# Optimization experiments

Measured on AMD Instinct MI355X. Metric: run time of the kernel, lower is better.

The kernel has to match this reference:

```python
import jax, jax.numpy as jnp
import numpy as np

NT, NRV, NR = 100000, 200000, 300000  # tile / road_vertex / road node counts
E = 400000                             # edges per edge type
B, H, P, A = 64, 128, 64, 512          # graphs, hidden, player_state_dim, action_dim


def _gat(h_src, h_dst, src, dst, W, a_s, a_d, b, n_dst):
    # PyG GATConv, heads=1, shared lin for src/dst, no self loops (bipartite)
    hs = h_src @ W                      # [Ns, H]
    hd = h_dst @ W                      # [Nd, H]
    e = jax.nn.leaky_relu((hs @ a_s)[src] + (hd @ a_d)[dst], 0.2)  # [E]
    m = jax.ops.segment_max(e, dst, num_segments=n_dst)
    w = jnp.exp(e - m[dst])
    denom = jax.ops.segment_sum(w, dst, num_segments=n_dst)
    alpha = w / jnp.maximum(denom[dst], 1e-16)                      # segment softmax
    out = jax.ops.segment_sum(alpha[:, None] * hs[src], dst, num_segments=n_dst)
    return out + b


def _mean_pool(x, batch, nb):
    s = jax.ops.segment_sum(x, batch, num_segments=nb)
    c = jax.ops.segment_sum(jnp.ones((x.shape[0],), x.dtype), batch, num_segments=nb)
    return s / jnp.maximum(c, 1.0)[:, None]


def setup_inputs():
    ks = iter(jax.random.split(jax.random.key(0), 64))
    f32 = jnp.float32

    def lin(i, o):
        return (jax.random.normal(next(ks), (i, o), f32) / np.float32(np.sqrt(i)))

    d = {}
    d['x_tile'] = jax.random.normal(next(ks), (NT, 8), f32)
    d['x_rv'] = jax.random.normal(next(ks), (NRV, 13), f32)
    d['x_road'] = jax.random.normal(next(ks), (NR, 4), f32)
    d['x_player'] = jax.random.normal(next(ks), (B, P), f32)
    # node encoders
    d['enc_t_W'] = lin(8, H);  d['enc_t_b'] = jnp.zeros((H,), f32)
    d['enc_rv_W'] = lin(13, H); d['enc_rv_b'] = jnp.zeros((H,), f32)
    d['enc_r_W'] = lin(4, H);  d['enc_r_b'] = jnp.zeros((H,), f32)
    # six GAT convs
    for name in ['rv2t', 't2rv', 'r2rv', 'rv2r', 't2r', 'r2t']:
        d[name + '_W'] = lin(H, H)
        d[name + '_as'] = jax.random.normal(next(ks), (H,), f32) * 0.1
        d[name + '_ad'] = jax.random.normal(next(ks), (H,), f32) * 0.1
        d[name + '_b'] = jnp.zeros((H,), f32)
    # player MLP + output head (input: 3H pooled + H player)
    d['fc1_W'] = lin(P, H); d['fc1_b'] = jnp.zeros((H,), f32)
    d['fc2_W'] = lin(H, H); d['fc2_b'] = jnp.zeros((H,), f32)
    d['out_W'] = lin(4 * H, A); d['out_b'] = jnp.zeros((A,), f32)
    # edges (src bounded by source-type count, dst by dest-type count)
    ri = lambda n, hi: jax.random.randint(n, (E,), 0, hi, jnp.int32)
    d['e_rv2t_src'] = ri(next(ks), NRV); d['e_rv2t_dst'] = ri(next(ks), NT)
    d['e_t2rv_src'] = ri(next(ks), NT);  d['e_t2rv_dst'] = ri(next(ks), NRV)
    d['e_r2rv_src'] = ri(next(ks), NR);  d['e_r2rv_dst'] = ri(next(ks), NRV)
    d['e_rv2r_src'] = ri(next(ks), NRV); d['e_rv2r_dst'] = ri(next(ks), NR)
    d['e_t2r_src'] = ri(next(ks), NT);   d['e_t2r_dst'] = ri(next(ks), NR)
    d['e_r2t_src'] = ri(next(ks), NR);   d['e_r2t_dst'] = ri(next(ks), NT)
    # batch assignment per node type
    d['batch_tile'] = jnp.sort(jax.random.randint(next(ks), (NT,), 0, B, jnp.int32))
    d['batch_rv'] = jnp.sort(jax.random.randint(next(ks), (NRV,), 0, B, jnp.int32))
    d['batch_road'] = jnp.sort(jax.random.randint(next(ks), (NR,), 0, B, jnp.int32))
    return d


def reference(x_tile, x_rv, x_road, x_player,
              enc_t_W, enc_t_b, enc_rv_W, enc_rv_b, enc_r_W, enc_r_b,
              rv2t_W, rv2t_as, rv2t_ad, rv2t_b,
              t2rv_W, t2rv_as, t2rv_ad, t2rv_b,
              r2rv_W, r2rv_as, r2rv_ad, r2rv_b,
              rv2r_W, rv2r_as, rv2r_ad, rv2r_b,
              t2r_W, t2r_as, t2r_ad, t2r_b,
              r2t_W, r2t_as, r2t_ad, r2t_b,
              fc1_W, fc1_b, fc2_W, fc2_b, out_W, out_b,
              e_rv2t_src, e_rv2t_dst, e_t2rv_src, e_t2rv_dst,
              e_r2rv_src, e_r2rv_dst, e_rv2r_src, e_rv2r_dst,
              e_t2r_src, e_t2r_dst, e_r2t_src, e_r2t_dst,
              batch_tile, batch_rv, batch_road):
    # node encoders
    h_t = x_tile @ enc_t_W + enc_t_b
    h_rv = x_rv @ enc_rv_W + enc_rv_b
    h_r = x_road @ enc_r_W + enc_r_b
    # hetero GAT, aggr='sum' over edge types per destination node type
    o_t = (_gat(h_rv, h_t, e_rv2t_src, e_rv2t_dst, rv2t_W, rv2t_as, rv2t_ad, rv2t_b, NT)
           + _gat(h_r, h_t, e_r2t_src, e_r2t_dst, r2t_W, r2t_as, r2t_ad, r2t_b, NT))
    o_rv = (_gat(h_t, h_rv, e_t2rv_src, e_t2rv_dst, t2rv_W, t2rv_as, t2rv_ad, t2rv_b, NRV)
            + _gat(h_r, h_rv, e_r2rv_src, e_r2rv_dst, r2rv_W, r2rv_as, r2rv_ad, r2rv_b, NRV))
    o_r = (_gat(h_rv, h_r, e_rv2r_src, e_rv2r_dst, rv2r_W, rv2r_as, rv2r_ad, rv2r_b, NR)
           + _gat(h_t, h_r, e_t2r_src, e_t2r_dst, t2r_W, t2r_as, t2r_ad, t2r_b, NR))
    # global mean pool per node type, concat -> [B, 3H]
    x_all = jnp.concatenate([_mean_pool(o_t, batch_tile, B),
                             _mean_pool(o_rv, batch_rv, B),
                             _mean_pool(o_r, batch_road, B)], axis=1)
    # player branch
    p = jax.nn.relu(x_player @ fc1_W + fc1_b)
    p = jax.nn.relu(p @ fc2_W + fc2_b)
    x = jnp.concatenate([x_all, p], axis=1)  # [B, 4H]
    return x @ out_W + out_b                 # [B, A]
```

## Files before the change

kernel.cpp:

```cpp
#include <hip/hip_runtime.h>


constexpr int kNT = 100000, kNRV = 200000, kNR = 300000, kE = 400000;
constexpr int kEq   = kE / 4;
constexpr int kSLOT = 1088;
constexpr int kNBB  = 1536;
constexpr int kBPS  = 192;
constexpr int kTOTD = 1200000;

constexpr long long OFF_C    = 0;
constexpr long long OFF_VS   = 13056;
constexpr long long OFF_VD   = 13176;
constexpr long long OFF_BD   = 13296;
constexpr long long OFF_PS   = 13512;
constexpr long long OFF_XCAT = 22216;
constexpr long long OFF_LS16 = 54984;
constexpr long long OFF_LD16 = 654984;
constexpr long long OFF_W16  = 1254984;
constexpr long long OFF_DN   = 2454984;
constexpr long long OFF_XR   = 3654984;
constexpr long long OFF_BID  = 6254984;
constexpr long long OFF_PB   = 6554984;

__constant__ const int kLSB[6]  = {0, 200000, 300000, 600000, 800000, 900000};
__constant__ const int kDRB[6]  = {0, 100000, 300000, 500000, 800000, 1100000};
__constant__ const int kDLEN[6] = {100000, 200000, 200000, 300000, 300000, 100000};
__constant__ const int cSlotEt[8]  = {1, 2, 4, 5, 0, 0, 3, 3};
__constant__ const int cSlotLo[8]  = {0, 0, 0, 0, 0, 100000, 0, 100000};
__constant__ const int cSlotHi[8]  = {1 << 30, 1 << 30, 1 << 30, 1 << 30,
                                      100000, 200000, 100000, 200000};
__constant__ const int cSlotCnt[8] = {1, 1, 1, 1, 1, 0, 1, 0};

__device__ __forceinline__ int lowb(const int* a, int n, int v) {
  int lo = 0, hi = n;
  while (lo < hi) { int mid = (lo + hi) >> 1; if (a[mid] < v) lo = mid + 1; else hi = mid; }
  return lo;
}

__global__ __launch_bounds__(256) void precompute_kernel(
    const float* encW_t, const float* encb_t,
    const float* encW_rv, const float* encb_rv,
    const float* encW_r, const float* encb_r,
    const float* W0, const float* as0, const float* ad0,
    const float* W1, const float* as1, const float* ad1,
    const float* W2, const float* as2, const float* ad2,
    const float* W3, const float* as3, const float* ad3,
    const float* W4, const float* as4, const float* ad4,
    const float* W5, const float* as5, const float* ad5,
    const int* bt, const int* brv, const int* br,
    float* Cws, float* vsw, float* vdw, int* BD)
{
  int tid = threadIdx.x;
  if (blockIdx.x == 24) {
    if (tid < 3 * 65) {
      int tt = tid / 65, q = tid - tt * 65;
      const int* ba = (tt == 0) ? bt : (tt == 1 ? brv : br);
      int N = (tt == 0) ? kNT : (tt == 1 ? kNRV : kNR);
      BD[tt * 72 + q] = lowb(ba, N, q);
    }
    return;
  }
  const float* encW[3] = {encW_t, encW_rv, encW_r};
  const float* encb[3] = {encb_t, encb_rv, encb_r};
  const int    Ks[3]   = {8, 13, 4};
  const float* Wv[6]  = {W0, W1, W2, W3, W4, W5};
  const float* asv[6] = {as0, as1, as2, as3, as4, as5};
  const float* adv[6] = {ad0, ad1, ad2, ad3, ad4, ad5};
  const int srcT[6] = {1, 0, 2, 1, 0, 2};
  const int dstT[6] = {0, 1, 1, 2, 2, 0};

  int et = blockIdx.x >> 2;
  int jc = blockIdx.x & 3;
  int st = srcT[et], dt = dstT[et];
  const float* eW = encW[st];
  const float* eB = encb[st];
  int K = Ks[st];
  const float* W = Wv[et];

  float* Cslot = Cws + et * 2176;
  for (int idx = tid; idx < (K + 1) * 32; idx += 256) {
    int r = idx >> 5, jj = idx & 31;
    int j = jc * 32 + jj;
    const float* row = (r < K) ? (eW + r * 128) : eB;
    float acc = 0.f;
    for (int m = 0; m < 128; ++m) acc += row[m] * W[m * 128 + j];
    Cslot[(r < K) ? (r * 128 + j) : (2048 + j)] = acc;
  }

  if (jc == 0) {
    __shared__ float us[128], wvs[128];
    const float* a_s = asv[et];
    const float* a_d = adv[et];
    if (tid < 128) {
      float acc = 0.f;
      for (int j = 0; j < 128; ++j) acc += W[tid * 128 + j] * a_s[j];
      us[tid] = acc;
    } else {
      int m = tid - 128;
      float acc = 0.f;
      for (int j = 0; j < 128; ++j) acc += W[m * 128 + j] * a_d[j];
      wvs[m] = acc;
    }
    __syncthreads();
    if (tid <= K) {
      const float* row = (tid < K) ? (eW + tid * 128) : eB;
      float acc = 0.f;
      for (int m = 0; m < 128; ++m) acc += row[m] * us[m];
      vsw[et * 20 + (tid < K ? tid : 16)] = acc;
    }
    int KD = Ks[dt];
    if (tid >= 32 && tid <= 32 + KD) {
      int k = tid - 32;
      const float* row = (k < KD) ? (encW[dt] + k * 128) : encb[dt];
      float acc = 0.f;
      for (int m = 0; m < 128; ++m) acc += row[m] * wvs[m];
      vdw[et * 20 + (k < KD ? k : 16)] = acc;
    }
  }
}

template <int K, int RH>
__device__ __forceinline__ void prep_one(
    const float* __restrict__ xr, unsigned char b,
    const float* __restrict__ vsA, const float* __restrict__ vsB,
    const float* __restrict__ vdA, const float* __restrict__ vdB,
    _Float16* lsA, _Float16* lsB, _Float16* ldA, _Float16* ldB,
    float* dnA, float* dnB, unsigned char* bidA, unsigned char* bidB,
    _Float16* xrec)
{
  float a0 = 0.f, a1 = 0.f, a2 = 0.f, a3 = 0.f;
#pragma unroll
  for (int k = 0; k < K; ++k) {
    float xv = xr[k];
    a0 += xv * vsA[k]; a1 += xv * vsB[k];
    a2 += xv * vdA[k]; a3 += xv * vdB[k];
    xrec[k] = (_Float16)xv;
  }
#pragma unroll
  for (int k = K; k < RH; ++k) xrec[k] = (_Float16)0.f;
  *lsA = (_Float16)(a0 + vsA[16]);
  *lsB = (_Float16)(a1 + vsB[16]);
  *ldA = (_Float16)(a2 + vdA[16]);
  *ldB = (_Float16)(a3 + vdB[16]);
  *dnA = 0.f;
  *dnB = 0.f;
  *bidA = b;
  *bidB = b;
}

__global__ __launch_bounds__(256) void prep_kernel(
    const float* __restrict__ x_t, const float* __restrict__ x_rv,
    const float* __restrict__ x_r,
    const int* __restrict__ bt, const int* __restrict__ brv,
    const int* __restrict__ br,
    const float* __restrict__ vsw, const float* __restrict__ vdw,
    _Float16* __restrict__ LS16, _Float16* __restrict__ LD16,
    float* __restrict__ DN, unsigned char* __restrict__ BID,
    _Float16* __restrict__ XR)
{
  int n = blockIdx.x * 256 + threadIdx.x;
  if (n >= kNT + kNRV + kNR) return;
  if (n < kNT) {
    prep_one<8, 8>(x_t + n * 8, (unsigned char)bt[n],
                   vsw + 1 * 20, vsw + 4 * 20, vdw + 0 * 20, vdw + 5 * 20,
                   LS16 + 200000 + n, LS16 + 800000 + n,
                   LD16 + 0 + n, LD16 + 1100000 + n,
                   DN + 0 + n, DN + 1100000 + n,
                   BID + 0 + n, BID + 1100000 + n,
                   XR + (long long)n * 8);
  } else if (n < kNT + kNRV) {
    int m = n - kNT;
    prep_one<13, 16>(x_rv + m * 13, (unsigned char)brv[m],
                     vsw + 0 * 20, vsw + 3 * 20, vdw + 1 * 20, vdw + 2 * 20,
                     LS16 + 0 + m, LS16 + 600000 + m,
                     LD16 + 100000 + m, LD16 + 300000 + m,
                     DN + 100000 + m, DN + 300000 + m,
                     BID + 100000 + m, BID + 300000 + m,
                     XR + 800000 + (long long)m * 16);
  } else {
    int m = n - kNT - kNRV;
    prep_one<4, 4>(x_r + m * 4, (unsigned char)br[m],
                   vsw + 2 * 20, vsw + 5 * 20, vdw + 3 * 20, vdw + 4 * 20,
                   LS16 + 300000 + m, LS16 + 900000 + m,
                   LD16 + 500000 + m, LD16 + 800000 + m,
                   DN + 500000 + m, DN + 800000 + m,
                   BID + 500000 + m, BID + 800000 + m,
                   XR + 4000000 + (long long)m * 4);
  }
}

__global__ __launch_bounds__(256) void passA_kernel(
    const int* s0, const int* s1, const int* s2,
    const int* s3, const int* s4, const int* s5,
    const int* d0, const int* d1, const int* d2,
    const int* d3, const int* d4, const int* d5,
    const _Float16* __restrict__ LS16, const _Float16* __restrict__ LD16,
    float* __restrict__ DN, _Float16* __restrict__ W16)
{
  int slot = blockIdx.x & 7;
  int blk = blockIdx.x >> 3;
  for (int i = blk * 256 + (int)threadIdx.x; i < 75000; i += kBPS * 256) {
    int gq = slot * 75000 + i;
    int et = gq / 100000;
    int q = gq - et * 100000;
    const int* sp; const int* dp;
    switch (et) {
      case 0: sp = s0; dp = d0; break;
      case 1: sp = s1; dp = d1; break;
      case 2: sp = s2; dp = d2; break;
      case 3: sp = s3; dp = d3; break;
      case 4: sp = s4; dp = d4; break;
      default: sp = s5; dp = d5; break;
    }
    int lsb = kLSB[et], drb = kDRB[et];
    int4 ss = ((const int4*)sp)[q];
    int4 dd = ((const int4*)dp)[q];
    int sa[4] = {ss.x, ss.y, ss.z, ss.w};
    int da[4] = {dd.x, dd.y, dd.z, dd.w};
    union { float2 f; _Float16 h[4]; } WU;
    float wa[4];
#pragma unroll
    for (int j = 0; j < 4; ++j) {
      float t = (float)LS16[lsb + sa[j]] + (float)LD16[drb + da[j]];
      t = t > 0.f ? t : 0.2f * t;
      _Float16 h = (_Float16)__expf(t);
      WU.h[j] = h;
      wa[j] = (float)h;
    }
    ((float2*)(W16 + (long long)et * kE))[q] = WU.f;
#pragma unroll
    for (int j = 0; j < 4; ++j) unsafeAtomicAdd(&DN[drb + da[j]], wa[j]);
  }
}

__global__ __launch_bounds__(256) void pack_kernel(
    const float* __restrict__ DN, const unsigned char* __restrict__ BID,
    unsigned* __restrict__ DNu)
{
  int j = blockIdx.x * 256 + threadIdx.x;
  if (j >= kTOTD) return;
  float dn = DN[j];
  unsigned u = 0u;
  if (dn > 0.f)
    u = (__float_as_uint(1.f / dn) & ~63u) | (unsigned)BID[j];
  DNu[j] = u;
}

template <int RH>
__device__ __forceinline__ void loadX(const _Float16* __restrict__ xp, float* xv) {
  if constexpr (RH == 4) {
    union { uint2 u; _Float16 h[4]; } U;
    U.u = *(const uint2*)xp;
#pragma unroll
    for (int k = 0; k < RH; ++k) xv[k] = (float)U.h[k];
  } else if constexpr (RH == 8) {
    union { uint4 u; _Float16 h[8]; } U;
    U.u = *(const uint4*)xp;
#pragma unroll
    for (int k = 0; k < RH; ++k) xv[k] = (float)U.h[k];
  } else {
    union { uint4 u[2]; _Float16 h[16]; } U;
    U.u[0] = *(const uint4*)xp;
    U.u[1] = *(const uint4*)(xp + 8);
#pragma unroll
    for (int k = 0; k < RH; ++k) xv[k] = (float)U.h[k];
  }
}

template <int K, int RH>
__device__ __forceinline__ void passB_loop(
    const int* __restrict__ sp, const int* __restrict__ dp,
    const _Float16* __restrict__ Wet, const unsigned* __restrict__ DNu, int drb,
    const _Float16* __restrict__ XR, long long xrb,
    float* __restrict__ lp, int lo, int hi, int start, int stride)
{
  for (int q = start; q < kEq; q += stride) {
    int4 ss = ((const int4*)sp)[q];
    int4 dd = ((const int4*)dp)[q];
    union { float2 f; _Float16 h[4]; } WU;
    WU.f = ((const float2*)Wet)[q];
    int sa[4] = {ss.x, ss.y, ss.z, ss.w};
    int da[4] = {dd.x, dd.y, dd.z, dd.w};
#pragma unroll
    for (int i = 0; i < 4; ++i) {
      int s = sa[i], d = da[i];
      if (s >= lo && s < hi) {
        unsigned u = DNu[drb + d];
        int b = (int)(u & 63u);
        float rinv = __uint_as_float(u & ~63u);
        float alpha = (float)WU.h[i] * rinv;
        float xv[RH];
        loadX<RH>(XR + xrb + (long long)s * RH, xv);
#pragma unroll
        for (int k = 0; k < K; ++k) atomicAdd(lp + k * 64 + b, alpha * xv[k]);
      }
    }
  }
}

__global__ __launch_bounds__(256) void passB_kernel(
    const int* s0, const int* s1, const int* s2,
    const int* s3, const int* s4, const int* s5,
    const int* d0, const int* d1, const int* d2,
    const int* d3, const int* d4, const int* d5,
    const _Float16* __restrict__ W16, const unsigned* __restrict__ DNu,
    const _Float16* __restrict__ XR, float* __restrict__ PB)
{
  __shared__ float lp[kSLOT];
  int tid = threadIdx.x;
  for (int j = tid; j < kSLOT; j += 256) lp[j] = 0.f;
  __syncthreads();
  int slot = blockIdx.x & 7;
  int blk = blockIdx.x >> 3;
  int et = cSlotEt[slot];
  int lo = cSlotLo[slot], hi = cSlotHi[slot];
  int start = blk * 256 + tid;
  int stride = kBPS * 256;
  int drb = kDRB[et];
  const _Float16* Wet = W16 + (long long)et * kE;
  switch (et) {
    case 0: passB_loop<13, 16>(s0, d0, Wet, DNu, drb, XR, 800000,  lp, lo, hi, start, stride); break;
    case 1: passB_loop< 8,  8>(s1, d1, Wet, DNu, drb, XR, 0,       lp, lo, hi, start, stride); break;
    case 2: passB_loop< 4,  4>(s2, d2, Wet, DNu, drb, XR, 4000000, lp, lo, hi, start, stride); break;
    case 3: passB_loop<13, 16>(s3, d3, Wet, DNu, drb, XR, 800000,  lp, lo, hi, start, stride); break;
    case 4: passB_loop< 8,  8>(s4, d4, Wet, DNu, drb, XR, 0,       lp, lo, hi, start, stride); break;
    default: passB_loop<4,  4>(s5, d5, Wet, DNu, drb, XR, 4000000, lp, lo, hi, start, stride); break;
  }
  if (cSlotCnt[slot]) {
    int dlen = kDLEN[et];
    for (int j = start; j < dlen; j += stride) {
      unsigned u = DNu[drb + j];
      if (u >> 6) atomicAdd(lp + 1024 + (int)(u & 63u), 1.f);
    }
  }
  __syncthreads();
  float* dst = PB + (long long)blockIdx.x * kSLOT;
  for (int j = tid; j < kSLOT; j += 256) dst[j] = lp[j];
}

__global__ __launch_bounds__(256) void reduce1_kernel(
    const float* __restrict__ PB, float* __restrict__ PS)
{
  int slot = blockIdx.x / 5;
  int jb = blockIdx.x - slot * 5;
  int j = jb * 256 + threadIdx.x;
  if (j >= kSLOT) return;
  float s = 0.f;
#pragma unroll 8
  for (int blk = 0; blk < kBPS; ++blk)
    s += PB[(long long)(blk * 8 + slot) * kSLOT + j];
  PS[slot * kSLOT + j] = s;
}

__global__ __launch_bounds__(128) void finalize_kernel(
    const int* __restrict__ BDg,
    const float* __restrict__ xp,
    const float* __restrict__ fc1W, const float* __restrict__ fc1b,
    const float* __restrict__ fc2W, const float* __restrict__ fc2b,
    const float* __restrict__ b_rv2t, const float* __restrict__ b_r2t,
    const float* __restrict__ b_t2rv, const float* __restrict__ b_r2rv,
    const float* __restrict__ b_rv2r, const float* __restrict__ b_t2r,
    const float* __restrict__ Cws, const float* __restrict__ PS,
    float* __restrict__ xcat)
{
  int b = blockIdx.x, tid = threadIdx.x;
  __shared__ float xps[64];
  __shared__ float p1s[128];
  if (tid < 64) xps[tid] = xp[b * 64 + tid];
  __syncthreads();
  float a = fc1b[tid];
  for (int k = 0; k < 64; ++k) a += xps[k] * fc1W[k * 128 + tid];
  p1s[tid] = fmaxf(a, 0.f);
  __syncthreads();
  float a2 = fc2b[tid];
  for (int k = 0; k < 128; ++k) a2 += p1s[k] * fc2W[k * 128 + tid];
  xcat[b * 512 + 384 + tid] = fmaxf(a2, 0.f);

  const int etA[3] = {0, 1, 3}, etB[3] = {5, 2, 4};
  const int KAv[3] = {13, 8, 13}, KBv[3] = {4, 4, 8};
  const int slotA[6] = {4, 0, 1, 6, 2, 3};
  const int slotB[6] = {5, -1, -1, 7, -1, -1};
  for (int t3 = 0; t3 < 3; ++t3) {
    int eA = etA[t3], eB = etB[t3];
    const float* CA = Cws + eA * 2176;
    const float* CB = Cws + eB * 2176;
    int sA1 = slotA[eA], sA2 = slotB[eA];
    int sB1 = slotA[eB], sB2 = slotB[eB];
    const float* PA1 = PS + sA1 * kSLOT;
    const float* PA2 = (sA2 >= 0) ? (PS + sA2 * kSLOT) : nullptr;
    const float* PB1 = PS + sB1 * kSLOT;
    const float* PB2 = (sB2 >= 0) ? (PS + sB2 * kSLOT) : nullptr;
    float cA = PA1[1024 + b] + (PA2 ? PA2[1024 + b] : 0.f);
    float cB = PB1[1024 + b] + (PB2 ? PB2[1024 + b] : 0.f);
    float v = cA * CA[2048 + tid] + cB * CB[2048 + tid];
    for (int k = 0; k < KAv[t3]; ++k) {
      float pv = PA1[k * 64 + b] + (PA2 ? PA2[k * 64 + b] : 0.f);
      v += pv * CA[k * 128 + tid];
    }
    for (int k = 0; k < KBv[t3]; ++k) {
      float pv = PB1[k * 64 + b] + (PB2 ? PB2[k * 64 + b] : 0.f);
      v += pv * CB[k * 128 + tid];
    }
    int cnt = BDg[t3 * 72 + b + 1] - BDg[t3 * 72 + b];
    float cntf = (float)max(cnt, 1);
    const float* bb1 = (t3 == 0) ? b_rv2t : (t3 == 1 ? b_t2rv : b_rv2r);
    const float* bb2 = (t3 == 0) ? b_r2t  : (t3 == 1 ? b_r2rv : b_t2r);
    xcat[b * 512 + t3 * 128 + tid] = v / cntf + bb1[tid] + bb2[tid];
  }
}

__global__ __launch_bounds__(256) void out_kernel(
    const float* __restrict__ xcat, const float* __restrict__ outW,
    const float* __restrict__ outb, float* __restrict__ out)
{
  int g = blockIdx.x * 256 + threadIdx.x;
  int r = g >> 9, c = g & 511;
  const float* xr = xcat + r * 512;
  float acc = outb[c];
  for (int k = 0; k < 512; ++k) acc += xr[k] * outW[k * 512 + c];
  out[g] = acc;
}

extern "C" void kernel_launch(void* const* d_in, const int* in_sizes, int n_in,
                              void* d_out, int out_size, void* d_ws, size_t ws_size,
                              hipStream_t stream) {
  const float* x_tile   = (const float*)d_in[0];
  const float* x_rv     = (const float*)d_in[1];
  const float* x_road   = (const float*)d_in[2];
  const float* x_player = (const float*)d_in[3];
  const float* enc_t_W  = (const float*)d_in[4];
  const float* enc_t_b  = (const float*)d_in[5];
  const float* enc_rv_W = (const float*)d_in[6];
  const float* enc_rv_b = (const float*)d_in[7];
  const float* enc_r_W  = (const float*)d_in[8];
  const float* enc_r_b  = (const float*)d_in[9];
  const float* W[6]; const float* As[6]; const float* Ad[6]; const float* Bb[6];
  for (int et = 0; et < 6; ++et) {
    W[et]  = (const float*)d_in[10 + 4 * et];
    As[et] = (const float*)d_in[11 + 4 * et];
    Ad[et] = (const float*)d_in[12 + 4 * et];
    Bb[et] = (const float*)d_in[13 + 4 * et];
  }
  const float* fc1W = (const float*)d_in[34];
  const float* fc1b = (const float*)d_in[35];
  const float* fc2W = (const float*)d_in[36];
  const float* fc2b = (const float*)d_in[37];
  const float* outW = (const float*)d_in[38];
  const float* outb = (const float*)d_in[39];
  const int* esrc[6]; const int* edst[6];
  for (int et = 0; et < 6; ++et) {
    esrc[et] = (const int*)d_in[40 + 2 * et];
    edst[et] = (const int*)d_in[41 + 2 * et];
  }
  const int* batch_t  = (const int*)d_in[52];
  const int* batch_rv = (const int*)d_in[53];
  const int* batch_r  = (const int*)d_in[54];

  float* wsF = (float*)d_ws;
  float* Cws  = wsF + OFF_C;
  float* vsw  = wsF + OFF_VS;
  float* vdw  = wsF + OFF_VD;
  int*   BD   = (int*)(wsF + OFF_BD);
  float* PS   = wsF + OFF_PS;
  float* xcat = wsF + OFF_XCAT;
  _Float16* LS16 = (_Float16*)(wsF + OFF_LS16);
  _Float16* LD16 = (_Float16*)(wsF + OFF_LD16);
  _Float16* W16 = (_Float16*)(wsF + OFF_W16);
  float* DN   = wsF + OFF_DN;
  unsigned* DNu = (unsigned*)(wsF + OFF_DN);
  _Float16* XR = (_Float16*)(wsF + OFF_XR);
  unsigned char* BID = (unsigned char*)(wsF + OFF_BID);
  float* PB   = wsF + OFF_PB;
  float* out  = (float*)d_out;

  precompute_kernel<<<25, 256, 0, stream>>>(
      enc_t_W, enc_t_b, enc_rv_W, enc_rv_b, enc_r_W, enc_r_b,
      W[0], As[0], Ad[0], W[1], As[1], Ad[1], W[2], As[2], Ad[2],
      W[3], As[3], Ad[3], W[4], As[4], Ad[4], W[5], As[5], Ad[5],
      batch_t, batch_rv, batch_r,
      Cws, vsw, vdw, BD);

  prep_kernel<<<(kNT + kNRV + kNR + 255) / 256, 256, 0, stream>>>(
      x_tile, x_rv, x_road, batch_t, batch_rv, batch_r, vsw, vdw,
      LS16, LD16, DN, BID, XR);

  passA_kernel<<<kNBB, 256, 0, stream>>>(
      esrc[0], esrc[1], esrc[2], esrc[3], esrc[4], esrc[5],
      edst[0], edst[1], edst[2], edst[3], edst[4], edst[5],
      LS16, LD16, DN, W16);

  pack_kernel<<<(kTOTD + 255) / 256, 256, 0, stream>>>(DN, BID, DNu);

  passB_kernel<<<kNBB, 256, 0, stream>>>(
      esrc[0], esrc[1], esrc[2], esrc[3], esrc[4], esrc[5],
      edst[0], edst[1], edst[2], edst[3], edst[4], edst[5],
      W16, DNu, XR, PB);

  reduce1_kernel<<<40, 256, 0, stream>>>(PB, PS);

  finalize_kernel<<<64, 128, 0, stream>>>(
      BD, x_player,
      fc1W, fc1b, fc2W, fc2b,
      Bb[0], Bb[5], Bb[1], Bb[2], Bb[3], Bb[4],
      Cws, PS, xcat);

  out_kernel<<<128, 256, 0, stream>>>(xcat, outW, outb, out);

  (void)in_sizes; (void)n_in; (void)out_size; (void)ws_size;
}
```

Baseline: 556.1 us.

## Partition edge passes by edge type with 256 blocks each, use nontemporal loads

Replaces the 8-slot work split, in which heavy edge types were split by source-index range and filtered per edge, with a plain 6 edge-types × 256 blocks grid. Each block now processes only its own type's edges without the lo/hi range check, and the reduction and finalize kernels are simplified to 6 partial slots. Streaming edge-index and weight loads and stores use nontemporal hints to avoid polluting cache. The cost is that load balance across edge types with different feature widths (13 vs 4) becomes uneven, since the old slotting split the wide types in two.

```diff
diff --git a/kernel.cpp b/kernel.cpp
--- a/kernel.cpp
+++ b/kernel.cpp
@@ -5,8 +5,10 @@
 constexpr int kEq   = kE / 4;
 constexpr int kSLOT = 1088;
 constexpr int kNBB  = 1536;
-constexpr int kBPS  = 192;
 constexpr int kTOTD = 1200000;
+
+typedef int   i4v __attribute__((ext_vector_type(4)));
+typedef float f2v __attribute__((ext_vector_type(2)));
 
 constexpr long long OFF_C    = 0;
 constexpr long long OFF_VS   = 13056;
@@ -25,11 +27,6 @@
 __constant__ const int kLSB[6]  = {0, 200000, 300000, 600000, 800000, 900000};
 __constant__ const int kDRB[6]  = {0, 100000, 300000, 500000, 800000, 1100000};
 __constant__ const int kDLEN[6] = {100000, 200000, 200000, 300000, 300000, 100000};
-__constant__ const int cSlotEt[8]  = {1, 2, 4, 5, 0, 0, 3, 3};
-__constant__ const int cSlotLo[8]  = {0, 0, 0, 0, 0, 100000, 0, 100000};
-__constant__ const int cSlotHi[8]  = {1 << 30, 1 << 30, 1 << 30, 1 << 30,
-                                      100000, 200000, 100000, 200000};
-__constant__ const int cSlotCnt[8] = {1, 1, 1, 1, 1, 0, 1, 0};
 
 __device__ __forceinline__ int lowb(const int* a, int n, int v) {
   int lo = 0, hi = n;
@@ -197,27 +194,25 @@
     const _Float16* __restrict__ LS16, const _Float16* __restrict__ LD16,
     float* __restrict__ DN, _Float16* __restrict__ W16)
 {
-  int slot = blockIdx.x & 7;
-  int blk = blockIdx.x >> 3;
-  for (int i = blk * 256 + (int)threadIdx.x; i < 75000; i += kBPS * 256) {
-    int gq = slot * 75000 + i;
-    int et = gq / 100000;
-    int q = gq - et * 100000;
-    const int* sp; const int* dp;
-    switch (et) {
-      case 0: sp = s0; dp = d0; break;
-      case 1: sp = s1; dp = d1; break;
-      case 2: sp = s2; dp = d2; break;
-      case 3: sp = s3; dp = d3; break;
-      case 4: sp = s4; dp = d4; break;
-      default: sp = s5; dp = d5; break;
-    }
-    int lsb = kLSB[et], drb = kDRB[et];
-    int4 ss = ((const int4*)sp)[q];
-    int4 dd = ((const int4*)dp)[q];
+  int et = blockIdx.x >> 8;
+  int blk = blockIdx.x & 255;
+  const int* sp; const int* dp;
+  switch (et) {
+    case 0: sp = s0; dp = d0; break;
+    case 1: sp = s1; dp = d1; break;
+    case 2: sp = s2; dp = d2; break;
+    case 3: sp = s3; dp = d3; break;
+    case 4: sp = s4; dp = d4; break;
+    default: sp = s5; dp = d5; break;
+  }
+  int lsb = kLSB[et], drb = kDRB[et];
+  f2v* Wet = (f2v*)(W16 + (long long)et * kE);
+  for (int q = blk * 256 + (int)threadIdx.x; q < kEq; q += 256 * 256) {
+    i4v ss = __builtin_nontemporal_load(((const i4v*)sp) + q);
+    i4v dd = __builtin_nontemporal_load(((const i4v*)dp) + q);
     int sa[4] = {ss.x, ss.y, ss.z, ss.w};
     int da[4] = {dd.x, dd.y, dd.z, dd.w};
-    union { float2 f; _Float16 h[4]; } WU;
+    union { f2v f; _Float16 h[4]; } WU;
     float wa[4];
 #pragma unroll
     for (int j = 0; j < 4; ++j) {
@@ -227,7 +222,7 @@
       WU.h[j] = h;
       wa[j] = (float)h;
     }
-    ((float2*)(W16 + (long long)et * kE))[q] = WU.f;
+    __builtin_nontemporal_store(WU.f, Wet + q);
 #pragma unroll
     for (int j = 0; j < 4; ++j) unsafeAtomicAdd(&DN[drb + da[j]], wa[j]);
   }
@@ -272,28 +267,26 @@
     const int* __restrict__ sp, const int* __restrict__ dp,
     const _Float16* __restrict__ Wet, const unsigned* __restrict__ DNu, int drb,
     const _Float16* __restrict__ XR, long long xrb,
-    float* __restrict__ lp, int lo, int hi, int start, int stride)
+    float* __restrict__ lp, int start, int stride)
 {
   for (int q = start; q < kEq; q += stride) {
-    int4 ss = ((const int4*)sp)[q];
-    int4 dd = ((const int4*)dp)[q];
-    union { float2 f; _Float16 h[4]; } WU;
-    WU.f = ((const float2*)Wet)[q];
+    i4v ss = __builtin_nontemporal_load(((const i4v*)sp) + q);
+    i4v dd = __builtin_nontemporal_load(((const i4v*)dp) + q);
+    union { f2v f; _Float16 h[4]; } WU;
+    WU.f = __builtin_nontemporal_load(((const f2v*)Wet) + q);
     int sa[4] = {ss.x, ss.y, ss.z, ss.w};
     int da[4] = {dd.x, dd.y, dd.z, dd.w};
 #pragma unroll
     for (int i = 0; i < 4; ++i) {
       int s = sa[i], d = da[i];
-      if (s >= lo && s < hi) {
-        unsigned u = DNu[drb + d];
-        int b = (int)(u & 63u);
-        float rinv = __uint_as_float(u & ~63u);
-        float alpha = (float)WU.h[i] * rinv;
-        float xv[RH];
-        loadX<RH>(XR + xrb + (long long)s * RH, xv);
-#pragma unroll
-        for (int k = 0; k < K; ++k) atomicAdd(lp + k * 64 + b, alpha * xv[k]);
-      }
+      unsigned u = DNu[drb + d];
+      int b = (int)(u & 63u);
+      float rinv = __uint_as_float(u & ~63u);
+      float alpha = (float)WU.h[i] * rinv;
+      float xv[RH];
+      loadX<RH>(XR + xrb + (long long)s * RH, xv);
+#pragma unroll
+      for (int k = 0; k < K; ++k) atomicAdd(lp + k * 64 + b, alpha * xv[k]);
     }
   }
 }
@@ -310,23 +303,21 @@
   int tid = threadIdx.x;
   for (int j = tid; j < kSLOT; j += 256) lp[j] = 0.f;
   __syncthreads();
-  int slot = blockIdx.x & 7;
-  int blk = blockIdx.x >> 3;
-  int et = cSlotEt[slot];
-  int lo = cSlotLo[slot], hi = cSlotHi[slot];
+  int et = blockIdx.x >> 8;
+  int blk = blockIdx.x & 255;
   int start = blk * 256 + tid;
-  int stride = kBPS * 256;
+  int stride = 256 * 256;
   int drb = kDRB[et];
   const _Float16* Wet = W16 + (long long)et * kE;
   switch (et) {
-    case 0: passB_loop<13, 16>(s0, d0, Wet, DNu, drb, XR, 800000,  lp, lo, hi, start, stride); break;
-    case 1: passB_loop< 8,  8>(s1, d1, Wet, DNu, drb, XR, 0,       lp, lo, hi, start, stride); break;
-    case 2: passB_loop< 4,  4>(s2, d2, Wet, DNu, drb, XR, 4000000, lp, lo, hi, start, stride); break;
-    case 3: passB_loop<13, 16>(s3, d3, Wet, DNu, drb, XR, 800000,  lp, lo, hi, start, stride); break;
-    case 4: passB_loop< 8,  8>(s4, d4, Wet, DNu, drb, XR, 0,       lp, lo, hi, start, stride); break;
-    default: passB_loop<4,  4>(s5, d5, Wet, DNu, drb, XR, 4000000, lp, lo, hi, start, stride); break;
-  }
-  if (cSlotCnt[slot]) {
+    case 0: passB_loop<13, 16>(s0, d0, Wet, DNu, drb, XR, 800000,  lp, start, stride); break;
+    case 1: passB_loop< 8,  8>(s1, d1, Wet, DNu, drb, XR, 0,       lp, start, stride); break;
+    case 2: passB_loop< 4,  4>(s2, d2, Wet, DNu, drb, XR, 4000000, lp, start, stride); break;
+    case 3: passB_loop<13, 16>(s3, d3, Wet, DNu, drb, XR, 800000,  lp, start, stride); break;
+    case 4: passB_loop< 8,  8>(s4, d4, Wet, DNu, drb, XR, 0,       lp, start, stride); break;
+    default: passB_loop<4,  4>(s5, d5, Wet, DNu, drb, XR, 4000000, lp, start, stride); break;
+  }
+  {
     int dlen = kDLEN[et];
     for (int j = start; j < dlen; j += stride) {
       unsigned u = DNu[drb + j];
@@ -335,21 +326,23 @@
   }
   __syncthreads();
   float* dst = PB + (long long)blockIdx.x * kSLOT;
-  for (int j = tid; j < kSLOT; j += 256) dst[j] = lp[j];
+  for (int j = tid; j < kSLOT; j += 256)
+    __builtin_nontemporal_store(lp[j], dst + j);
 }
 
 __global__ __launch_bounds__(256) void reduce1_kernel(
     const float* __restrict__ PB, float* __restrict__ PS)
 {
-  int slot = blockIdx.x / 5;
-  int jb = blockIdx.x - slot * 5;
+  int et = blockIdx.x / 5;
+  int jb = blockIdx.x - et * 5;
   int j = jb * 256 + threadIdx.x;
   if (j >= kSLOT) return;
+  const float* base = PB + (long long)(et * 256) * kSLOT + j;
   float s = 0.f;
 #pragma unroll 8
-  for (int blk = 0; blk < kBPS; ++blk)
-    s += PB[(long long)(blk * 8 + slot) * kSLOT + j];
-  PS[slot * kSLOT + j] = s;
+  for (int blk = 0; blk < 256; ++blk)
+    s += base[(long long)blk * kSLOT];
+  PS[et * kSLOT + j] = s;
 }
 
 __global__ __launch_bounds__(128) void finalize_kernel(
@@ -378,29 +371,17 @@
 
   const int etA[3] = {0, 1, 3}, etB[3] = {5, 2, 4};
   const int KAv[3] = {13, 8, 13}, KBv[3] = {4, 4, 8};
-  const int slotA[6] = {4, 0, 1, 6, 2, 3};
-  const int slotB[6] = {5, -1, -1, 7, -1, -1};
   for (int t3 = 0; t3 < 3; ++t3) {
     int eA = etA[t3], eB = etB[t3];
     const float* CA = Cws + eA * 2176;
     const float* CB = Cws + eB * 2176;
-    int sA1 = slotA[eA], sA2 = slotB[eA];
-    int sB1 = slotA[eB], sB2 = slotB[eB];
-    const float* PA1 = PS + sA1 * kSLOT;
-    const float* PA2 = (sA2 >= 0) ? (PS + sA2 * kSLOT) : nullptr;
-    const float* PB1 = PS + sB1 * kSLOT;
-    const float* PB2 = (sB2 >= 0) ? (PS + sB2 * kSLOT) : nullptr;
-    float cA = PA1[1024 + b] + (PA2 ? PA2[1024 + b] : 0.f);
-    float cB = PB1[1024 + b] + (PB2 ? PB2[1024 + b] : 0.f);
+    const float* pA = PS + eA * kSLOT;
+    const float* pB = PS + eB * kSLOT;
+    float cA = pA[1024 + b];
+    float cB = pB[1024 + b];
     float v = cA * CA[2048 + tid] + cB * CB[2048 + tid];
-    for (int k = 0; k < KAv[t3]; ++k) {
-      float pv = PA1[k * 64 + b] + (PA2 ? PA2[k * 64 + b] : 0.f);
-      v += pv * CA[k * 128 + tid];
-    }
-    for (int k = 0; k < KBv[t3]; ++k) {
-      float pv = PB1[k * 64 + b] + (PB2 ? PB2[k * 64 + b] : 0.f);
-      v += pv * CB[k * 128 + tid];
-    }
+    for (int k = 0; k < KAv[t3]; ++k) v += pA[k * 64 + b] * CA[k * 128 + tid];
+    for (int k = 0; k < KBv[t3]; ++k) v += pB[k * 64 + b] * CB[k * 128 + tid];
     int cnt = BDg[t3 * 72 + b + 1] - BDg[t3 * 72 + b];
     float cntf = (float)max(cnt, 1);
     const float* bb1 = (t3 == 0) ? b_rv2t : (t3 == 1 ? b_t2rv : b_rv2r);
@@ -496,7 +477,7 @@
       edst[0], edst[1], edst[2], edst[3], edst[4], edst[5],
       W16, DNu, XR, PB);
 
-  reduce1_kernel<<<40, 256, 0, stream>>>(PB, PS);
+  reduce1_kernel<<<30, 256, 0, stream>>>(PB, PS);
 
   finalize_kernel<<<64, 128, 0, stream>>>(
       BD, x_player,
```

Result: no change. 555.5 us (-0.1%).
